# Optimization experiments

Measured on AMD Instinct MI355X. Metric: run time of the kernel, lower is better.

Reference implementation:

```python
import jax, jax.numpy as jnp
import numpy as np
import math

T = 1024        # num tokens
HIDDEN = 2880
HD = 64         # head_dim
NH = 64         # attention heads
NKV = 8         # kv heads
SW = 128        # sliding window (layer_idx=0 -> even -> active)
QKV_DIM = HD * (NH + 2 * NKV)  # 5120


def _rope_cos_sin(num_tokens):
    # YaRN (NTK-by-parts) rotary tables; all constants from ModelConfig defaults.
    base = 150000.0; scaling = 32.0; init_ctx = 4096.0
    ntk_alpha = 1.0; ntk_beta = 32.0
    d_half = HD / 2
    freq = base ** (np.arange(0, HD, 2, dtype=np.float32) / HD)
    concentration = 0.1 * math.log(scaling) + 1.0
    low = d_half * math.log(init_ctx / (ntk_beta * 2 * math.pi)) / math.log(base)
    high = d_half * math.log(init_ctx / (ntk_alpha * 2 * math.pi)) / math.log(base)
    interpolation = 1.0 / (scaling * freq)
    extrapolation = 1.0 / freq
    ramp = (np.arange(int(d_half), dtype=np.float32) - low) / (high - low)
    m = 1.0 - np.clip(ramp, 0.0, 1.0)
    inv_freq = interpolation * (1.0 - m) + extrapolation * m
    t = np.arange(num_tokens, dtype=np.float32)
    freqs = t[:, None] * inv_freq[None, :]
    cos = (np.cos(freqs) * concentration).astype(np.float32)
    sin = (np.sin(freqs) * concentration).astype(np.float32)
    return jnp.asarray(cos), jnp.asarray(sin)  # [T, HD//2]


def _apply_rope(x, cos, sin):
    # x: [T, H, HD]; cos/sin: [T, 1, HD//2]
    half = x.shape[-1] // 2
    x1, x2 = x[..., :half], x[..., half:]
    return jnp.concatenate([x1 * cos - x2 * sin, x2 * cos + x1 * sin], axis=-1)


def setup_inputs() -> dict:
    key = jax.random.key(0)
    ks = jax.random.split(key, 7)
    return {
        "x": jax.random.normal(ks[0], (T, HIDDEN), jnp.float32),
        "norm_scale": jnp.ones((HIDDEN,), jnp.float32),
        "qkv_w": jax.random.normal(ks[1], (QKV_DIM, HIDDEN), jnp.float32) / math.sqrt(HIDDEN),
        "qkv_b": jax.random.normal(ks[2], (QKV_DIM,), jnp.float32) * 0.02,
        "out_w": jax.random.normal(ks[3], (HIDDEN, NH * HD), jnp.float32) / math.sqrt(NH * HD),
        "out_b": jax.random.normal(ks[4], (HIDDEN,), jnp.float32) * 0.02,
        "sinks": jax.random.normal(ks[5], (NH,), jnp.float32),
    }


def reference(x, norm_scale, qkv_w, qkv_b, out_w, out_b, sinks):
    # --- RMSNorm ---
    t = x * jax.lax.rsqrt(jnp.mean(x * x, axis=-1, keepdims=True) + 1e-5) * norm_scale
    # --- fused QKV projection ---
    qkv = t @ qkv_w.T + qkv_b                      # [T, 5120]
    q_end = NH * HD
    k_end = q_end + NKV * HD
    q = qkv[:, :q_end].reshape(T, NH, HD)
    k = qkv[:, q_end:k_end].reshape(T, NKV, HD)
    v = qkv[:, k_end:].reshape(T, NKV, HD)
    # --- RoPE (YaRN) ---
    cos, sin = _rope_cos_sin(T)
    cos = cos[:, None, :]; sin = sin[:, None, :]   # [T, 1, HD//2]
    q = _apply_rope(q, cos, sin)
    k = _apply_rope(k, cos, sin)
    # --- GQA expand ---
    groups = NH // NKV
    k_e = jnp.repeat(k, groups, axis=1)            # [T, NH, HD]
    v_e = jnp.repeat(v, groups, axis=1)
    # --- scores + causal & sliding-window mask ---
    sm_scale = 1.0 / math.sqrt(HD)
    QK = jnp.einsum('qhd,khd->hqk', q, k_e) * sm_scale  # [NH, T, T]
    qi = jnp.arange(T)
    ki = jnp.arange(T)
    mask = (qi[:, None] < ki[None, :]) | (qi[:, None] >= ki[None, :] + SW)
    QK = jnp.where(mask[None], -jnp.inf, QK)
    # --- learned per-head sink logit appended to the softmax ---
    sink_col = jnp.broadcast_to(sinks[:, None, None], (NH, T, 1))
    logits = jnp.concatenate([QK, sink_col], axis=-1)   # [NH, T, T+1]
    W = jax.nn.softmax(logits, axis=-1)[..., :-1]       # drop sink prob
    # --- weighted values + output projection ---
    attn = jnp.einsum('hqk,khd->qhd', W, v_e)            # [T, NH, HD]
    return attn.reshape(T, NH * HD) @ out_w.T + out_b    # [T, HIDDEN]
```

## Files before the change

### kernel.cpp

```cpp
#include <hip/hip_runtime.h>
#include <hip/hip_bf16.h>
#include <math.h>

#define T_TOK 1024
#define HIDDEN 2880
#define HD 64
#define NH 64
#define NKV 8
#define SW 128
#define QKV_DIM 5120
#define ATTN_DIM 4096
#define OW_NPAD 2944

typedef __attribute__((ext_vector_type(8))) short sv8;
typedef __attribute__((ext_vector_type(8))) _Float16 h8;
typedef __attribute__((ext_vector_type(4))) float f32x4;

__device__ __forceinline__ ushort f2bf(float f) {
    union { float f; unsigned u; } v; v.f = f;
    unsigned r = v.u + 0x7fffu + ((v.u >> 16) & 1u);
    return (ushort)(r >> 16);
}
__device__ __forceinline__ float bf2f(ushort h) {
    union { unsigned u; float f; } v; v.u = ((unsigned)h) << 16;
    return v.f;
}
__device__ __forceinline__ void gload16(const ushort* g, ushort* l) {
    __builtin_amdgcn_global_load_lds(
        (const __attribute__((address_space(1))) unsigned int*)g,
        (__attribute__((address_space(3))) unsigned int*)l, 16, 0, 0);
}

__global__ void rope_table_kernel(float* __restrict__ cosT, float* __restrict__ sinT) {
    int gid = blockIdx.x * 256 + threadIdx.x;
    int i = gid & 31;
    int t = gid >> 5;
    const double d_half = 32.0;
    double freq = pow(150000.0, (double)i / 32.0);
    double lowd  = d_half * log(4096.0 / (32.0 * 2.0 * M_PI)) / log(150000.0);
    double highd = d_half * log(4096.0 / (2.0 * M_PI)) / log(150000.0);
    double ramp = ((double)i - lowd) / (highd - lowd);
    ramp = fmin(fmax(ramp, 0.0), 1.0);
    double m = 1.0 - ramp;
    double inv_freq = (1.0 / (32.0 * freq)) * (1.0 - m) + (1.0 / freq) * m;
    float phase = (float)t * (float)inv_freq;
    double conc = 0.1 * log(32.0) + 1.0;
    cosT[gid] = (float)(cos((double)phase) * conc);
    sinT[gid] = (float)(sin((double)phase) * conc);
}

__global__ __launch_bounds__(256) void split_kernel(const float* __restrict__ X,
                                                    ushort* __restrict__ hi,
                                                    ushort* __restrict__ lo,
                                                    long n_src, long n_dst) {
    long i = ((long)blockIdx.x * 256 + threadIdx.x) * 4;
    if (i >= n_dst) return;
    float4 v = make_float4(0.f, 0.f, 0.f, 0.f);
    if (i < n_src) v = *(const float4*)(X + i);
    ushort4 h, l;
    h.x = f2bf(v.x); l.x = f2bf(v.x - bf2f(h.x));
    h.y = f2bf(v.y); l.y = f2bf(v.y - bf2f(h.y));
    h.z = f2bf(v.z); l.z = f2bf(v.z - bf2f(h.z));
    h.w = f2bf(v.w); l.w = f2bf(v.w - bf2f(h.w));
    *(ushort4*)(hi + i) = h;
    *(ushort4*)(lo + i) = l;
}

__global__ __launch_bounds__(256) void rmsnorm_kernel(const float* __restrict__ x,
                                                      const float* __restrict__ scale,
                                                      ushort* __restrict__ t_hi,
                                                      ushort* __restrict__ t_lo) {
    const int row = blockIdx.x;
    const int tid = threadIdx.x;
    const float4* xr = (const float4*)(x + (size_t)row * HIDDEN);
    float4 v[3];
    float ss = 0.f;
    int cnt = 0;
    for (int i = tid; i < HIDDEN / 4; i += 256) {
        float4 a = xr[i];
        v[cnt++] = a;
        ss += a.x * a.x + a.y * a.y + a.z * a.z + a.w * a.w;
    }
    #pragma unroll
    for (int off = 32; off; off >>= 1) ss += __shfl_xor(ss, off);
    __shared__ float red[4];
    if ((tid & 63) == 0) red[tid >> 6] = ss;
    __syncthreads();
    float total = red[0] + red[1] + red[2] + red[3];
    float inv = rsqrtf(total / (float)HIDDEN + 1e-5f);
    const float4* sc = (const float4*)scale;
    cnt = 0;
    for (int i = tid; i < HIDDEN / 4; i += 256) {
        float4 a = v[cnt++];
        float4 s4 = sc[i];
        float4 o;
        o.x = a.x * inv * s4.x; o.y = a.y * inv * s4.y;
        o.z = a.z * inv * s4.z; o.w = a.w * inv * s4.w;
        ushort4 h, l;
        h.x = f2bf(o.x); l.x = f2bf(o.x - bf2f(h.x));
        h.y = f2bf(o.y); l.y = f2bf(o.y - bf2f(h.y));
        h.z = f2bf(o.z); l.z = f2bf(o.z - bf2f(h.z));
        h.w = f2bf(o.w); l.w = f2bf(o.w - bf2f(h.w));
        *(ushort4*)(t_hi + (size_t)row * HIDDEN + i * 4) = h;
        *(ushort4*)(t_lo + (size_t)row * HIDDEN + i * 4) = l;
    }
}

__global__ __launch_bounds__(256) void gemm_mfma_split(
    const ushort* __restrict__ Ahi, const ushort* __restrict__ Alo,
    const ushort* __restrict__ Bhi, const ushort* __restrict__ Blo,
    const float* __restrict__ bias, float* __restrict__ C,
    const int N, const int K)
{
    __shared__ __align__(16) ushort sAhi[128 * 64];
    __shared__ __align__(16) ushort sAlo[128 * 64];
    __shared__ __align__(16) ushort sBhi[128 * 64];
    __shared__ __align__(16) ushort sBlo[128 * 64];

    const int tid = threadIdx.x;
    const int m0 = blockIdx.x * 128;
    const int n0 = blockIdx.y * 128;
    const int w = tid >> 6, lane = tid & 63;
    const int wr = (w >> 1) * 64, wc = (w & 1) * 64;
    const int fr = lane & 15, fq = lane >> 4;

    int offA[4], offB[4], loff[4];
    #pragma unroll
    for (int q = 0; q < 4; ++q) {
        int c = tid + q * 256;
        int row = c >> 3, pc = c & 7;
        int gcol = (pc ^ (row & 7)) * 8;
        offA[q] = (m0 + row) * K + gcol;
        offB[q] = (n0 + row) * K + gcol;
        loff[q] = c * 8;
    }

    f32x4 acc[4][4] = {};

    for (int k0 = 0; k0 < K; k0 += 64) {
        #pragma unroll
        for (int q = 0; q < 4; ++q) {
            gload16(Ahi + offA[q] + k0, sAhi + loff[q]);
            gload16(Alo + offA[q] + k0, sAlo + loff[q]);
            gload16(Bhi + offB[q] + k0, sBhi + loff[q]);
            gload16(Blo + offB[q] + k0, sBlo + loff[q]);
        }
        __syncthreads();
        #pragma unroll
        for (int ks = 0; ks < 2; ++ks) {
            sv8 ahi[4], alo[4], bhi[4], blo[4];
            const int cx = ((ks * 4 + fq) ^ (fr & 7)) * 8;
            #pragma unroll
            for (int i = 0; i < 4; ++i) {
                int ra = (wr + i * 16 + fr) * 64 + cx;
                ahi[i] = *(const sv8*)(sAhi + ra);
                alo[i] = *(const sv8*)(sAlo + ra);
                int rb = (wc + i * 16 + fr) * 64 + cx;
                bhi[i] = *(const sv8*)(sBhi + rb);
                blo[i] = *(const sv8*)(sBlo + rb);
            }
            #pragma unroll
            for (int i = 0; i < 4; ++i)
                #pragma unroll
                for (int j = 0; j < 4; ++j) {
                    acc[i][j] = __builtin_amdgcn_mfma_f32_16x16x32_bf16(ahi[i], bhi[j], acc[i][j], 0, 0, 0);
                    acc[i][j] = __builtin_amdgcn_mfma_f32_16x16x32_bf16(ahi[i], blo[j], acc[i][j], 0, 0, 0);
                    acc[i][j] = __builtin_amdgcn_mfma_f32_16x16x32_bf16(alo[i], bhi[j], acc[i][j], 0, 0, 0);
                }
        }
        __syncthreads();
    }

    #pragma unroll
    for (int j = 0; j < 4; ++j) {
        int col = n0 + wc + j * 16 + fr;
        if (col < N) {
            float bv = bias[col];
            #pragma unroll
            for (int i = 0; i < 4; ++i) {
                int row = m0 + wr + i * 16 + fq * 4;
                #pragma unroll
                for (int r = 0; r < 4; ++r)
                    C[(size_t)(row + r) * N + col] = acc[i][j][r] + bv;
            }
        }
    }
}

__global__ __launch_bounds__(256) void rope_apply_kernel(float* __restrict__ qkv,
                                                         const float* __restrict__ cosT,
                                                         const float* __restrict__ sinT) {
    int gid = blockIdx.x * 256 + threadIdx.x;
    int i = gid & 31;
    int head = (gid >> 5) % 72;
    int t = gid / (72 * 32);
    size_t base = (size_t)t * QKV_DIM + (head < 64 ? head * 64 : ATTN_DIM + (head - 64) * 64);
    float x1 = qkv[base + i], x2 = qkv[base + 32 + i];
    float c = cosT[t * 32 + i], s = sinT[t * 32 + i];
    qkv[base + i]      = x1 * c - x2 * s;
    qkv[base + 32 + i] = x2 * c + x1 * s;
}

__global__ __launch_bounds__(256, 1) void attn_mfma_kernel(
    const float* __restrict__ qkv, const float* __restrict__ sinks,
    ushort* __restrict__ attn_hi, ushort* __restrict__ attn_lo)
{
    __shared__ __align__(16) char smem[122880];
    ushort*   Khi = (ushort*)smem;
    ushort*   Klo = (ushort*)(smem + 20480);
    _Float16* Wl  = (_Float16*)smem;
    _Float16* Vt  = (_Float16*)(smem + 98304);

    const int q0 = blockIdx.x * 32;
    const int g  = blockIdx.y;
    const int tid = threadIdx.x;
    const int w = tid >> 6, lane = tid & 63;
    const int fr = lane & 15, fq = lane >> 4;
    const int s0 = (q0 > 127) ? (q0 - 127) : 0;
    const int kmax = q0 + 32 - s0;

    for (int idx = tid; idx < 160 * 8; idx += 256) {
        int j = idx >> 3, c = idx & 7;
        float kv[8], vv[8];
        if (j < kmax) {
            const float* src = qkv + (size_t)(s0 + j) * QKV_DIM + ATTN_DIM + g * 64 + c * 8;
            *(float4*)&kv[0] = *(const float4*)src;
            *(float4*)&kv[4] = *(const float4*)(src + 4);
            const float* srcv = src + NKV * 64;
            *(float4*)&vv[0] = *(const float4*)srcv;
            *(float4*)&vv[4] = *(const float4*)(srcv + 4);
        } else {
            #pragma unroll
            for (int e = 0; e < 8; ++e) { kv[e] = 0.f; vv[e] = 0.f; }
        }
        sv8 hv, lv;
        #pragma unroll
        for (int e = 0; e < 8; ++e) {
            ushort h = f2bf(kv[e]);
            hv[e] = (short)h;
            lv[e] = (short)f2bf(kv[e] - bf2f(h));
        }
        int cs = c ^ (j & 7);
        *(sv8*)(Khi + j * 64 + cs * 8) = hv;
        *(sv8*)(Klo + j * 64 + cs * 8) = lv;
        int cj = j >> 3, jl = j & 7;
        #pragma unroll
        for (int e = 0; e < 8; ++e) {
            int d = c * 8 + e;
            int cp = (cj & 24) | ((cj & 7) ^ (d & 7));
            Vt[d * 192 + cp * 8 + jl] = (_Float16)vv[e];
        }
    }

    sv8 qhi[4][2], qlo[4][2];
    #pragma unroll
    for (int rf = 0; rf < 4; ++rf) {
        int hl = w * 2 + (rf >> 1);
        int qr = (rf & 1) * 16 + fr;
        const float* qrow = qkv + (size_t)(q0 + qr) * QKV_DIM + (g * 8 + hl) * 64;
        #pragma unroll
        for (int ks = 0; ks < 2; ++ks) {
            float v[8];
            *(float4*)&v[0] = *(const float4*)(qrow + ks * 32 + fq * 8);
            *(float4*)&v[4] = *(const float4*)(qrow + ks * 32 + fq * 8 + 4);
            #pragma unroll
            for (int e = 0; e < 8; ++e) {
                ushort h = f2bf(v[e]);
                qhi[rf][ks][e] = (short)h;
                qlo[rf][ks][e] = (short)f2bf(v[e] - bf2f(h));
            }
        }
    }

    __syncthreads();

    const int ncf = (kmax + 15) >> 4;
    f32x4 S[4][10] = {};
    #pragma unroll
    for (int ks = 0; ks < 2; ++ks) {
        #pragma unroll
        for (int cf = 0; cf < 10; ++cf) {
            if (cf < ncf) {
                int key = cf * 16 + fr;
                int cs = (ks * 4 + fq) ^ (key & 7);
                sv8 kh = *(const sv8*)(Khi + key * 64 + cs * 8);
                sv8 kl = *(const sv8*)(Klo + key * 64 + cs * 8);
                #pragma unroll
                for (int rf = 0; rf < 4; ++rf) {
                    S[rf][cf] = __builtin_amdgcn_mfma_f32_16x16x32_bf16(qhi[rf][ks], kh, S[rf][cf], 0, 0, 0);
                    S[rf][cf] = __builtin_amdgcn_mfma_f32_16x16x32_bf16(qlo[rf][ks], kh, S[rf][cf], 0, 0, 0);
                    S[rf][cf] = __builtin_amdgcn_mfma_f32_16x16x32_bf16(qhi[rf][ks], kl, S[rf][cf], 0, 0, 0);
                }
            }
        }
    }

    __syncthreads();

    float inv_s[4][4];
    #pragma unroll
    for (int rf = 0; rf < 4; ++rf) {
        float sink = sinks[g * 8 + w * 2 + (rf >> 1)];
        #pragma unroll
        for (int r = 0; r < 4; ++r) {
            int q = q0 + (rf & 1) * 16 + fq * 4 + r;
            float sv[10];
            float mx = sink;
            #pragma unroll
            for (int cf = 0; cf < 10; ++cf) {
                float v = S[rf][cf][r] * 0.125f;
                int kg = s0 + cf * 16 + fr;
                bool ok = (cf < ncf) && (kg <= q) && (kg + SW > q);
                v = ok ? v : -INFINITY;
                sv[cf] = v;
                mx = fmaxf(mx, v);
            }
            #pragma unroll
            for (int off = 1; off < 16; off <<= 1) mx = fmaxf(mx, __shfl_xor(mx, off));
            float sum = 0.f;
            #pragma unroll
            for (int cf = 0; cf < 10; ++cf) {
                float e = __expf(sv[cf] - mx);
                sv[cf] = e;
                sum += e;
            }
            #pragma unroll
            for (int off = 1; off < 16; off <<= 1) sum += __shfl_xor(sum, off);
            sum += __expf(sink - mx);
            inv_s[rf][r] = 1.f / sum;
            int row = w * 64 + rf * 16 + fq * 4 + r;
            #pragma unroll
            for (int cf = 0; cf < 10; ++cf) {
                if (cf < ncf) {
                    int key = cf * 16 + fr;
                    int cj = key >> 3;
                    int cp = (cj & 24) | ((cj & 7) ^ (row & 7));
                    Wl[row * 192 + cp * 8 + (key & 7)] = (_Float16)sv[cf];
                }
            }
        }
    }

    __syncthreads();

    const int nks = (kmax + 31) >> 5;
    f32x4 O[4][4] = {};
    #pragma unroll
    for (int ks = 0; ks < 5; ++ks) {
        if (ks < nks) {
            h8 a[4], b[4];
            int cj = ks * 4 + fq;
            #pragma unroll
            for (int rf = 0; rf < 4; ++rf) {
                int row = w * 64 + rf * 16 + fr;
                int cp = (cj & 24) | ((cj & 7) ^ (row & 7));
                a[rf] = *(const h8*)(Wl + row * 192 + cp * 8);
            }
            #pragma unroll
            for (int df = 0; df < 4; ++df) {
                int d = df * 16 + fr;
                int cp = (cj & 24) | ((cj & 7) ^ (d & 7));
                b[df] = *(const h8*)(Vt + d * 192 + cp * 8);
            }
            #pragma unroll
            for (int rf = 0; rf < 4; ++rf)
                #pragma unroll
                for (int df = 0; df < 4; ++df)
                    O[rf][df] = __builtin_amdgcn_mfma_f32_16x16x32_f16(a[rf], b[df], O[rf][df], 0, 0, 0);
        }
    }

    #pragma unroll
    for (int rf = 0; rf < 4; ++rf) {
        int H = g * 8 + w * 2 + (rf >> 1);
        #pragma unroll
        for (int df = 0; df < 4; ++df) {
            int d = df * 16 + fr;
            #pragma unroll
            for (int r = 0; r < 4; ++r) {
                int qr = (rf & 1) * 16 + fq * 4 + r;
                float v = O[rf][df][r] * inv_s[rf][r];
                size_t addr = (size_t)(q0 + qr) * ATTN_DIM + H * 64 + d;
                ushort h16 = f2bf(v);
                attn_hi[addr] = h16;
                attn_lo[addr] = f2bf(v - bf2f(h16));
            }
        }
    }
}

extern "C" void kernel_launch(void* const* d_in, const int* in_sizes, int n_in,
                              void* d_out, int out_size, void* d_ws, size_t ws_size,
                              hipStream_t stream) {
    const float* x          = (const float*)d_in[0];
    const float* norm_scale = (const float*)d_in[1];
    const float* qkv_w      = (const float*)d_in[2];
    const float* qkv_b      = (const float*)d_in[3];
    const float* out_w      = (const float*)d_in[4];
    const float* out_b      = (const float*)d_in[5];
    const float* sinks      = (const float*)d_in[6];
    float* out = (float*)d_out;

    char* p = (char*)d_ws;
    auto alloc = [&](size_t bytes) { char* r = p; p += (bytes + 255) & ~(size_t)255; return r; };
    const size_t W_ELEMS  = (size_t)QKV_DIM * HIDDEN;
    const size_t W_ELEMS2 = (size_t)OW_NPAD * ATTN_DIM;
    const size_t W_MAX = W_ELEMS > W_ELEMS2 ? W_ELEMS : W_ELEMS2;
    ushort* w_hi  = (ushort*)alloc(W_MAX * 2);
    ushort* w_lo  = (ushort*)alloc(W_MAX * 2);
    ushort* ab_hi  = (ushort*)alloc((size_t)T_TOK * ATTN_DIM * 2);
    ushort* ab_lo  = (ushort*)alloc((size_t)T_TOK * ATTN_DIM * 2);
    float*  qkv_buf = (float*)alloc((size_t)T_TOK * QKV_DIM * 4);
    float*  cosT   = (float*)alloc((size_t)T_TOK * 32 * 4);
    float*  sinT   = (float*)alloc((size_t)T_TOK * 32 * 4);

    rope_table_kernel<<<(T_TOK * 32) / 256, 256, 0, stream>>>(cosT, sinT);

    long n_qw = (long)QKV_DIM * HIDDEN;
    split_kernel<<<(int)(n_qw / 4 / 256), 256, 0, stream>>>(qkv_w, w_hi, w_lo, n_qw, n_qw);

    rmsnorm_kernel<<<T_TOK, 256, 0, stream>>>(x, norm_scale, ab_hi, ab_lo);

    gemm_mfma_split<<<dim3(T_TOK / 128, QKV_DIM / 128), 256, 0, stream>>>(
        ab_hi, ab_lo, w_hi, w_lo, qkv_b, qkv_buf, QKV_DIM, HIDDEN);

    rope_apply_kernel<<<(T_TOK * 72 * 32) / 256, 256, 0, stream>>>(qkv_buf, cosT, sinT);

    attn_mfma_kernel<<<dim3(T_TOK / 32, NKV), 256, 0, stream>>>(qkv_buf, sinks, ab_hi, ab_lo);

    long n_ow_src = (long)HIDDEN * ATTN_DIM;
    long n_ow_dst = (long)OW_NPAD * ATTN_DIM;
    split_kernel<<<(int)(n_ow_dst / 4 / 256), 256, 0, stream>>>(out_w, w_hi, w_lo, n_ow_src, n_ow_dst);

    gemm_mfma_split<<<dim3(T_TOK / 128, OW_NPAD / 128), 256, 0, stream>>>(
        ab_hi, ab_lo, w_hi, w_lo, out_b, out, HIDDEN, ATTN_DIM);
}
```

Measured before the change: 440.0 us.

## Fuse RoPE into QKV GEMM epilogue, shrink M tile, remap blocks for locality

Removes the separate rope_apply kernel by applying the rotary rotation in the QKV GEMM epilogue. Each warp holds both halves of a head (columns d and d+32) in its accumulators, so the rotation is done in registers before the store. The GEMM M tile shrinks from 128 to 64 rows with launch_bounds(256,2), which doubles the number of blocks and should raise occupancy. A 1D grid with a swizzled block-to-tile mapping is used to improve L2 reuse. The cost is less reuse of B per block, since each B tile now feeds only 64 rows, giving more global traffic for B.

```diff
diff --git a/kernel.cpp b/kernel.cpp
--- a/kernel.cpp
+++ b/kernel.cpp
@@ -11,6 +11,7 @@
 #define QKV_DIM 5120
 #define ATTN_DIM 4096
 #define OW_NPAD 2944
+#define ROPE_END 4608
 
 typedef __attribute__((ext_vector_type(8))) short sv8;
 typedef __attribute__((ext_vector_type(8))) _Float16 h8;
@@ -106,61 +107,80 @@
     }
 }
 
-__global__ __launch_bounds__(256) void gemm_mfma_split(
+template <bool ROPE>
+__global__ __launch_bounds__(256, 2) void gemm_mfma_split(
     const ushort* __restrict__ Ahi, const ushort* __restrict__ Alo,
     const ushort* __restrict__ Bhi, const ushort* __restrict__ Blo,
     const float* __restrict__ bias, float* __restrict__ C,
+    const float* __restrict__ cosT, const float* __restrict__ sinT,
     const int N, const int K)
 {
-    __shared__ __align__(16) ushort sAhi[128 * 64];
-    __shared__ __align__(16) ushort sAlo[128 * 64];
+    __shared__ __align__(16) ushort sAhi[64 * 64];
+    __shared__ __align__(16) ushort sAlo[64 * 64];
     __shared__ __align__(16) ushort sBhi[128 * 64];
     __shared__ __align__(16) ushort sBlo[128 * 64];
 
     const int tid = threadIdx.x;
-    const int m0 = blockIdx.x * 128;
-    const int n0 = blockIdx.y * 128;
+    const int cpx = gridDim.x >> 3;
+    const int L = blockIdx.x;
+    const int lin = (L & 7) * cpx + (L >> 3);
+    const int m0 = (lin & 15) * 64;
+    const int n0 = (lin >> 4) * 128;
+
     const int w = tid >> 6, lane = tid & 63;
-    const int wr = (w >> 1) * 64, wc = (w & 1) * 64;
+    const int wr = (w >> 1) * 32, wc = (w & 1) * 64;
     const int fr = lane & 15, fq = lane >> 4;
 
-    int offA[4], offB[4], loff[4];
+    int offA[2], loffA[2], offB[4], loffB[4];
+    #pragma unroll
+    for (int q = 0; q < 2; ++q) {
+        int c = tid + q * 256;
+        int row = c >> 3, pc = c & 7;
+        int gcol = (pc ^ (row & 7)) * 8;
+        offA[q] = (m0 + row) * K + gcol;
+        loffA[q] = c * 8;
+    }
     #pragma unroll
     for (int q = 0; q < 4; ++q) {
         int c = tid + q * 256;
         int row = c >> 3, pc = c & 7;
         int gcol = (pc ^ (row & 7)) * 8;
-        offA[q] = (m0 + row) * K + gcol;
         offB[q] = (n0 + row) * K + gcol;
-        loff[q] = c * 8;
-    }
-
-    f32x4 acc[4][4] = {};
+        loffB[q] = c * 8;
+    }
+
+    f32x4 acc[2][4] = {};
 
     for (int k0 = 0; k0 < K; k0 += 64) {
         #pragma unroll
+        for (int q = 0; q < 2; ++q) {
+            gload16(Ahi + offA[q] + k0, sAhi + loffA[q]);
+            gload16(Alo + offA[q] + k0, sAlo + loffA[q]);
+        }
+        #pragma unroll
         for (int q = 0; q < 4; ++q) {
-            gload16(Ahi + offA[q] + k0, sAhi + loff[q]);
-            gload16(Alo + offA[q] + k0, sAlo + loff[q]);
-            gload16(Bhi + offB[q] + k0, sBhi + loff[q]);
-            gload16(Blo + offB[q] + k0, sBlo + loff[q]);
+            gload16(Bhi + offB[q] + k0, sBhi + loffB[q]);
+            gload16(Blo + offB[q] + k0, sBlo + loffB[q]);
         }
         __syncthreads();
         #pragma unroll
         for (int ks = 0; ks < 2; ++ks) {
-            sv8 ahi[4], alo[4], bhi[4], blo[4];
+            sv8 ahi[2], alo[2], bhi[4], blo[4];
             const int cx = ((ks * 4 + fq) ^ (fr & 7)) * 8;
             #pragma unroll
-            for (int i = 0; i < 4; ++i) {
+            for (int i = 0; i < 2; ++i) {
                 int ra = (wr + i * 16 + fr) * 64 + cx;
                 ahi[i] = *(const sv8*)(sAhi + ra);
                 alo[i] = *(const sv8*)(sAlo + ra);
-                int rb = (wc + i * 16 + fr) * 64 + cx;
-                bhi[i] = *(const sv8*)(sBhi + rb);
-                blo[i] = *(const sv8*)(sBlo + rb);
-            }
-            #pragma unroll
-            for (int i = 0; i < 4; ++i)
+            }
+            #pragma unroll
+            for (int j = 0; j < 4; ++j) {
+                int rb = (wc + j * 16 + fr) * 64 + cx;
+                bhi[j] = *(const sv8*)(sBhi + rb);
+                blo[j] = *(const sv8*)(sBlo + rb);
+            }
+            #pragma unroll
+            for (int i = 0; i < 2; ++i)
                 #pragma unroll
                 for (int j = 0; j < 4; ++j) {
                     acc[i][j] = __builtin_amdgcn_mfma_f32_16x16x32_bf16(ahi[i], bhi[j], acc[i][j], 0, 0, 0);
@@ -171,34 +191,48 @@
         __syncthreads();
     }
 
-    #pragma unroll
-    for (int j = 0; j < 4; ++j) {
-        int col = n0 + wc + j * 16 + fr;
-        if (col < N) {
-            float bv = bias[col];
-            #pragma unroll
-            for (int i = 0; i < 4; ++i) {
-                int row = m0 + wr + i * 16 + fq * 4;
+    if (ROPE) {
+        const bool rope = (n0 + wc) < ROPE_END;
+        #pragma unroll
+        for (int j = 0; j < 2; ++j) {
+            const int col1 = n0 + wc + j * 16 + fr;
+            const int col2 = col1 + 32;
+            const float b1 = bias[col1], b2 = bias[col2];
+            const int d = j * 16 + fr;
+            #pragma unroll
+            for (int i = 0; i < 2; ++i) {
                 #pragma unroll
-                for (int r = 0; r < 4; ++r)
-                    C[(size_t)(row + r) * N + col] = acc[i][j][r] + bv;
-            }
-        }
-    }
-}
-
-__global__ __launch_bounds__(256) void rope_apply_kernel(float* __restrict__ qkv,
-                                                         const float* __restrict__ cosT,
-                                                         const float* __restrict__ sinT) {
-    int gid = blockIdx.x * 256 + threadIdx.x;
-    int i = gid & 31;
-    int head = (gid >> 5) % 72;
-    int t = gid / (72 * 32);
-    size_t base = (size_t)t * QKV_DIM + (head < 64 ? head * 64 : ATTN_DIM + (head - 64) * 64);
-    float x1 = qkv[base + i], x2 = qkv[base + 32 + i];
-    float c = cosT[t * 32 + i], s = sinT[t * 32 + i];
-    qkv[base + i]      = x1 * c - x2 * s;
-    qkv[base + 32 + i] = x2 * c + x1 * s;
+                for (int r = 0; r < 4; ++r) {
+                    int row = m0 + wr + i * 16 + fq * 4 + r;
+                    float v1 = acc[i][j][r] + b1;
+                    float v2 = acc[i][j + 2][r] + b2;
+                    if (rope) {
+                        float c = cosT[row * 32 + d], s = sinT[row * 32 + d];
+                        float w1 = v1 * c - v2 * s;
+                        float w2 = v2 * c + v1 * s;
+                        v1 = w1; v2 = w2;
+                    }
+                    C[(size_t)row * N + col1] = v1;
+                    C[(size_t)row * N + col2] = v2;
+                }
+            }
+        }
+    } else {
+        #pragma unroll
+        for (int j = 0; j < 4; ++j) {
+            int col = n0 + wc + j * 16 + fr;
+            if (col < N) {
+                float bv = bias[col];
+                #pragma unroll
+                for (int i = 0; i < 2; ++i) {
+                    int row = m0 + wr + i * 16 + fq * 4;
+                    #pragma unroll
+                    for (int r = 0; r < 4; ++r)
+                        C[(size_t)(row + r) * N + col] = acc[i][j][r] + bv;
+                }
+            }
+        }
+    }
 }
 
 __global__ __launch_bounds__(256, 1) void attn_mfma_kernel(
@@ -421,10 +455,8 @@
 
     rmsnorm_kernel<<<T_TOK, 256, 0, stream>>>(x, norm_scale, ab_hi, ab_lo);
 
-    gemm_mfma_split<<<dim3(T_TOK / 128, QKV_DIM / 128), 256, 0, stream>>>(
-        ab_hi, ab_lo, w_hi, w_lo, qkv_b, qkv_buf, QKV_DIM, HIDDEN);
-
-    rope_apply_kernel<<<(T_TOK * 72 * 32) / 256, 256, 0, stream>>>(qkv_buf, cosT, sinT);
+    gemm_mfma_split<true><<<(T_TOK / 64) * (QKV_DIM / 128), 256, 0, stream>>>(
+        ab_hi, ab_lo, w_hi, w_lo, qkv_b, qkv_buf, cosT, sinT, QKV_DIM, HIDDEN);
 
     attn_mfma_kernel<<<dim3(T_TOK / 32, NKV), 256, 0, stream>>>(qkv_buf, sinks, ab_hi, ab_lo);
 
@@ -432,6 +464,6 @@
     long n_ow_dst = (long)OW_NPAD * ATTN_DIM;
     split_kernel<<<(int)(n_ow_dst / 4 / 256), 256, 0, stream>>>(out_w, w_hi, w_lo, n_ow_src, n_ow_dst);
 
-    gemm_mfma_split<<<dim3(T_TOK / 128, OW_NPAD / 128), 256, 0, stream>>>(
-        ab_hi, ab_lo, w_hi, w_lo, out_b, out, HIDDEN, ATTN_DIM);
-}
+    gemm_mfma_split<false><<<(T_TOK / 64) * (OW_NPAD / 128), 256, 0, stream>>>(
+        ab_hi, ab_lo, w_hi, w_lo, out_b, out, nullptr, nullptr, HIDDEN, ATTN_DIM);
+}
```

Result: faster. 399.2 us (-9.3%).
